# Kernel tuning notes

Hardware: AMD Instinct MI355X
Metric: run time of the kernel (lower is better)

The kernel has to match this reference:

```python
import jax, jax.numpy as jnp
import numpy as np

B, L, F, C, H, FF = 8, 64, 16, 128, 8, 512


def setup_inputs() -> dict:
    key = jax.random.key(0)
    ks = jax.random.split(key, 5)
    s = jnp.float32(0.02)
    return {
        "x": jax.random.normal(ks[0], (B, L, F, C), jnp.float32),
        "wq": jax.random.normal(ks[1], (C * H, C), jnp.float32) * s,
        "bq": jnp.zeros((C * H,), jnp.float32),
        "wk": jax.random.normal(ks[2], (C * H, C), jnp.float32) * s,
        "bk": jnp.zeros((C * H,), jnp.float32),
        "wv": jax.random.normal(ks[3], (C * H, C), jnp.float32) * s,
        "bv": jnp.zeros((C * H,), jnp.float32),
        "wo": jax.random.normal(ks[4], (C, C * H), jnp.float32) * s,
        "bo": jnp.zeros((C,), jnp.float32),
        "ln1_g": jnp.ones((C,), jnp.float32),
        "ln1_b": jnp.zeros((C,), jnp.float32),
        "w1": jax.random.normal(jax.random.fold_in(key, 10), (FF, C), jnp.float32) * s,
        "b1": jnp.zeros((FF,), jnp.float32),
        "w2": jax.random.normal(jax.random.fold_in(key, 11), (C, FF), jnp.float32) * s,
        "b2": jnp.zeros((C,), jnp.float32),
        "ln2_g": jnp.ones((C,), jnp.float32),
        "ln2_b": jnp.zeros((C,), jnp.float32),
    }


def _layer_norm(x, g, b, eps=1e-5):
    m = jnp.mean(x, axis=-1, keepdims=True)
    v = jnp.mean(jnp.square(x - m), axis=-1, keepdims=True)  # biased var, like torch LN
    return (x - m) * jax.lax.rsqrt(v + eps) * g + b


def reference(x, wq, bq, wk, bk, wv, bv, wo, bo, ln1_g, ln1_b, w1, b1, w2, b2, ln2_g, ln2_b):
    b_, l, f, c = x.shape
    h = wq.shape[0] // c  # num_heads

    def proj(w, bias):
        y = x @ w.T + bias                       # (B,L,F,C*H)
        y = y.reshape(b_, l, f, c, h)
        return jnp.transpose(y, (0, 4, 1, 2, 3))  # (B,H,L,F,C)

    q = proj(wq, bq)
    k = proj(wk, bk)
    v = proj(wv, bv)

    # scores over joint (L,F) query/key axes: (B,H,Lq,Fq,Lk,Fk)
    scores = jnp.einsum('bhlfc,bhmgc->bhlfmg', q, k) / jnp.sqrt(jnp.float32(c))
    # double softmax: first over key-L axis, then over key-F axis of the result
    a = jax.nn.softmax(scores, axis=4)
    a = jax.nn.softmax(a, axis=5)
    z = jnp.einsum('bhlfmg,bhmgc->bhlfc', a, v)   # (B,H,L,F,C)
    z = jnp.transpose(z, (0, 2, 3, 4, 1)).reshape(b_, l, f, c * h)
    attn_out = z @ wo.T + bo                      # (B,L,F,C)

    z1 = _layer_norm(attn_out + x, ln1_g, ln1_b)  # residual + LN1 (dropout=0, eval)
    ffy = jax.nn.relu(z1 @ w1.T + b1) @ w2.T + b2
    return _layer_norm(ffy + z1, ln2_g, ln2_b)
```

## Files before the change

kernel.cpp:

```cpp
#include <hip/hip_runtime.h>


typedef unsigned short u16;
typedef unsigned int u32;
typedef __attribute__((ext_vector_type(4))) float f32x4;
typedef __attribute__((ext_vector_type(8))) short s16x8;
typedef __attribute__((ext_vector_type(4))) unsigned short u16x4;

__device__ __forceinline__ u16 f2bf(float f) {
    union { float f; u32 u; } v; v.f = f;
    u32 u = v.u;
    u += 0x7fffu + ((u >> 16) & 1u);
    return (u16)(u >> 16);
}
__device__ __forceinline__ float bf2f(u16 h) {
    union { u32 u; float f; } v; v.u = ((u32)h) << 16;
    return v.f;
}
__device__ __forceinline__ u32 pack_trunc(float lo, float hi) {
    return __builtin_amdgcn_perm(__float_as_uint(hi), __float_as_uint(lo), 0x07060302u);
}
__device__ __forceinline__ s16x8 ldg8(const u16* p) { return *(const s16x8*)p; }

#define MFMA(a, b, c) __builtin_amdgcn_mfma_f32_16x16x32_bf16((a), (b), (c), 0, 0, 0)

__global__ __launch_bounds__(256) void k_prep(
    const float* __restrict__ x, const float* __restrict__ wq,
    const float* __restrict__ wk, const float* __restrict__ wv,
    const float* __restrict__ wo, const float* __restrict__ w1,
    const float* __restrict__ w2,
    u16* __restrict__ Xb, u16* __restrict__ Wqb, u16* __restrict__ Wkb,
    u16* __restrict__ Wvb, u16* __restrict__ Wob, u16* __restrict__ W1b,
    u16* __restrict__ W2b)
{
    int i = blockIdx.x * 256 + threadIdx.x;
    if (i < 360448) {
        int v = i * 4;
        float4 f; u16* dst; size_t addr;
        if (v < 1048576) {
            int t = v >> 7, k = v & 127;
            f = *(const float4*)(x + v);
            dst = Xb;
            addr = (size_t)((t >> 4) * 4 + (k >> 5)) * 512 + (t & 15) * 32 + (k & 31);
        } else {
            int v2 = v - 1048576;
            int w = v2 >> 17, off = v2 & 131071;
            const float* src = (w == 0) ? wq : (w == 1) ? wk : wv;
            dst = (w == 0) ? Wqb : (w == 1) ? Wkb : Wvb;
            int o = off >> 7, k = off & 127;
            int h = o & 7, cp = o >> 3;
            f = *(const float4*)(src + off);
            addr = (size_t)((h * 8 + (cp >> 4)) * 4 + (k >> 5)) * 512 + (cp & 15) * 32 + (k & 31);
        }
        u16x4 o4; o4.x = f2bf(f.x); o4.y = f2bf(f.y); o4.z = f2bf(f.z); o4.w = f2bf(f.w);
        *(u16x4*)(dst + addr) = o4;
    } else {
        int i2 = i - 360448;
        if (i2 < 131072) {
            int n = i2 >> 10, o2 = i2 & 1023;
            int h = o2 >> 7, c = o2 & 127;
            size_t addr = (size_t)((n >> 4) * 32 + (o2 >> 5)) * 512 + (n & 15) * 32 + (o2 & 31);
            Wob[addr] = f2bf(wo[n * 1024 + c * 8 + h]);
        } else {
            int v = (i2 - 131072) * 4;
            float4 f; u16* dst; size_t addr;
            if (v < 65536) {
                int o = v >> 7, k = v & 127;
                f = *(const float4*)(w1 + v);
                dst = W1b;
                addr = (size_t)((o >> 4) * 4 + (k >> 5)) * 512 + (o & 15) * 32 + (k & 31);
            } else {
                int v2 = v - 65536;
                int n = v2 >> 9, k = v2 & 511;
                f = *(const float4*)(w2 + v2);
                dst = W2b;
                addr = (size_t)((n >> 4) * 16 + (k >> 5)) * 512 + (n & 15) * 32 + (k & 31);
            }
            u16x4 o4; o4.x = f2bf(f.x); o4.y = f2bf(f.y); o4.z = f2bf(f.z); o4.w = f2bf(f.w);
            *(u16x4*)(dst + addr) = o4;
        }
    }
}

__global__ __launch_bounds__(256) void k_qkv(
    const u16* __restrict__ Xb,
    const u16* __restrict__ Wqb, const u16* __restrict__ Wkb, const u16* __restrict__ Wvb,
    const float* __restrict__ bq, const float* __restrict__ bk, const float* __restrict__ bv,
    u16* __restrict__ Qblk, u16* __restrict__ Kblk, u16* __restrict__ Vblk)
{
    const int tid = threadIdx.x, lane = tid & 63, wid = tid >> 6;
    const int colb = lane & 15, quad = lane >> 4;
    const int fl = colb * 32 + quad * 8;
    const int t0 = blockIdx.x * 128;
    const int cb = blockIdx.y;
    const int h = cb >> 1, c0 = (cb & 1) * 64;

    const u16* at0 = Xb + (size_t)((t0 >> 4) + wid * 2) * 2048 + fl;
    const u16* at1 = at0 + 2048;
    s16x8 a0[4], a1[4];
    #pragma unroll
    for (int i = 0; i < 4; ++i) { a0[i] = ldg8(at0 + i * 512); a1[i] = ldg8(at1 + i * 512); }

    #pragma unroll
    for (int gz = 0; gz < 3; ++gz) {
        const u16* W = (gz == 0) ? Wqb : (gz == 1) ? Wkb : Wvb;
        const float* bias = (gz == 0) ? bq : (gz == 1) ? bk : bv;
        f32x4 acc[2][4] = {};
        #pragma unroll
        for (int j = 0; j < 4; ++j) {
            int cpt = (c0 >> 4) + j;
            const u16* bt = W + (size_t)((h * 8 + cpt) * 4) * 512 + fl;
            #pragma unroll
            for (int i = 0; i < 4; ++i) {
                s16x8 b = ldg8(bt + i * 512);
                acc[0][j] = MFMA(a0[i], b, acc[0][j]);
                acc[1][j] = MFMA(a1[i], b, acc[1][j]);
            }
        }
        #pragma unroll
        for (int rt = 0; rt < 2; ++rt) {
            #pragma unroll
            for (int j = 0; j < 4; ++j) {
                int cpr = c0 + j * 16 + colb;
                float bs = bias[cpr * 8 + h];
                if (gz < 2) {
                    u16* dst = (gz == 0) ? Qblk : Kblk;
                    #pragma unroll
                    for (int r = 0; r < 4; ++r) {
                        int t = t0 + (wid * 2 + rt) * 16 + quad * 4 + r;
                        int bi = t >> 10, rr = t & 1023;
                        size_t addr = (size_t)(bi * 8 + h) * 131072
                                    + (size_t)((rr >> 4) * 4 + (cpr >> 5)) * 512
                                    + (rr & 15) * 32 + (cpr & 31);
                        dst[addr] = f2bf(acc[rt][j][r] + bs);
                    }
                } else {
                    int t = t0 + (wid * 2 + rt) * 16 + quad * 4;
                    int bi = t >> 10, rr = t & 1023;
                    size_t addr = (size_t)(bi * 8 + h) * 131072
                                + (size_t)((cpr >> 4) * 32 + (rr >> 5)) * 512
                                + (cpr & 15) * 32 + (rr & 31);
                    u16x4 o;
                    o.x = f2bf(acc[rt][j][0] + bs); o.y = f2bf(acc[rt][j][1] + bs);
                    o.z = f2bf(acc[rt][j][2] + bs); o.w = f2bf(acc[rt][j][3] + bs);
                    *(u16x4*)&Vblk[addr] = o;
                }
            }
        }
    }
}

__global__ __launch_bounds__(512, 4) void k_attn(
    const u16* __restrict__ Qblk, const u16* __restrict__ Kblk, const u16* __restrict__ Vblk,
    u16* __restrict__ Zblk)
{
    __shared__ u16 sS[32 * 1032];
    __shared__ float sZsum[32][16];
    __shared__ float sZi[32][20];

    const int tid = threadIdx.x, lane = tid & 63, wid = tid >> 6;
    const int colb = lane & 15, quad = lane >> 4;
    const int fl = colb * 32 + quad * 8;
    const int bid = blockIdx.x;
    const int bh = (bid & 7) + 8 * ((bid >> 3) & 7);
    const int r0 = (bid >> 6) * 32;
    const size_t qkb = (size_t)bh * 131072;
    const float SCALE = 0.08838834764831845f;

    sZsum[tid >> 4][tid & 15] = 0.f;
    __syncthreads();

    const u16* qt = Qblk + qkb + (size_t)(r0 >> 4) * 2048 + fl;
    s16x8 aq[2][4];
    #pragma unroll
    for (int mt = 0; mt < 2; ++mt)
        #pragma unroll
        for (int i = 0; i < 4; ++i)
            aq[mt][i] = ldg8(qt + mt * 2048 + i * 512);

    const u16* kt0 = Kblk + qkb + (size_t)wid * 2048 + fl;
    float zs[2][4] = {};
    s16x8 kc[4], kn[4];
    #pragma unroll
    for (int i = 0; i < 4; ++i) kc[i] = ldg8(kt0 + i * 512);
    #pragma unroll
    for (int j = 0; j < 8; ++j) {
        if (j < 7) {
            const u16* kp = kt0 + (size_t)(8 * (j + 1)) * 2048;
            #pragma unroll
            for (int i = 0; i < 4; ++i) kn[i] = ldg8(kp + i * 512);
        }
        f32x4 ac0 = {}, ac1 = {};
        ac0 = MFMA(aq[0][0], kc[0], ac0); ac1 = MFMA(aq[1][0], kc[0], ac1);
        ac0 = MFMA(aq[0][1], kc[1], ac0); ac1 = MFMA(aq[1][1], kc[1], ac1);
        ac0 = MFMA(aq[0][2], kc[2], ac0); ac1 = MFMA(aq[1][2], kc[2], ac1);
        ac0 = MFMA(aq[0][3], kc[3], ac0); ac1 = MFMA(aq[1][3], kc[3], ac1);
        const int kt = wid + 8 * j;
        #pragma unroll
        for (int r = 0; r < 4; ++r) {
            int row0 = quad * 4 + r;
            float p0 = __expf(ac0[r] * SCALE);
            float p1 = __expf(ac1[r] * SCALE);
            u32 u0 = __float_as_uint(p0), u1 = __float_as_uint(p1);
            zs[0][r] += __uint_as_float(u0 & 0xffff0000u);
            zs[1][r] += __uint_as_float(u1 & 0xffff0000u);
            sS[row0 * 1032 + kt * 16 + colb] = (u16)(u0 >> 16);
            sS[(16 + row0) * 1032 + kt * 16 + colb] = (u16)(u1 >> 16);
        }
        #pragma unroll
        for (int i = 0; i < 4; ++i) kc[i] = kn[i];
    }
    #pragma unroll
    for (int mt = 0; mt < 2; ++mt)
        #pragma unroll
        for (int r = 0; r < 4; ++r)
            atomicAdd(&sZsum[mt * 16 + quad * 4 + r][colb], zs[mt][r]);
    __syncthreads();

    {
        int row = tid >> 4, g = tid & 15;
        sZi[row][g] = 1.0f / sZsum[row][g];
    }
    __syncthreads();

    {
        const int row = tid & 31, mb = (tid >> 5) * 4;
        float zi[16];
        #pragma unroll
        for (int i = 0; i < 4; ++i) {
            f32x4 z4 = *(const f32x4*)&sZi[row][i * 4];
            zi[i*4] = z4[0]; zi[i*4+1] = z4[1]; zi[i*4+2] = z4[2]; zi[i*4+3] = z4[3];
        }
        #pragma unroll
        for (int tk = 0; tk < 4; ++tk) {
            int m = mb + tk;
            u16* base = &sS[row * 1032 + m * 16];
            s16x8 pa = *(const s16x8*)base;
            s16x8 pb = *(const s16x8*)(base + 8);
            float w[16]; float sum = 0.f;
            #pragma unroll
            for (int g = 0; g < 8; ++g) {
                w[g] = __expf(bf2f((u16)pa[g]) * zi[g]);      sum += w[g];
                w[g+8] = __expf(bf2f((u16)pb[g]) * zi[g+8]);  sum += w[g+8];
            }
            float inv = 1.0f / sum;
            u32 o[8];
            #pragma unroll
            for (int g = 0; g < 8; ++g)
                o[g] = pack_trunc(w[2*g] * inv, w[2*g+1] * inv);
            *(u32*)(base + 0)  = o[0]; *(u32*)(base + 2)  = o[1];
            *(u32*)(base + 4)  = o[2]; *(u32*)(base + 6)  = o[3];
            *(u32*)(base + 8)  = o[4]; *(u32*)(base + 10) = o[5];
            *(u32*)(base + 12) = o[6]; *(u32*)(base + 14) = o[7];
        }
    }
    __syncthreads();

    f32x4 zac[2] = {};
    const u16* aS0 = &sS[colb * 1032 + quad * 8];
    const u16* aS1 = aS0 + 16 * 1032;
    const u16* vt = Vblk + qkb + (size_t)wid * 16384 + fl;
    #pragma unroll
    for (int c = 0; c < 8; ++c) {
        s16x8 v[4];
        #pragma unroll
        for (int i = 0; i < 4; ++i) v[i] = ldg8(vt + (c * 4 + i) * 512);
        #pragma unroll
        for (int i = 0; i < 4; ++i) {
            int kk = (c * 4 + i) * 32;
            zac[0] = MFMA(*(const s16x8*)(aS0 + kk), v[i], zac[0]);
            zac[1] = MFMA(*(const s16x8*)(aS1 + kk), v[i], zac[1]);
        }
    }
    const int bi = bh >> 3, hh = bh & 7;
    const int tt = (bi * 1024 + r0) >> 4;
    #pragma unroll
    for (int mt = 0; mt < 2; ++mt) {
        size_t base = (size_t)((tt + mt) * 32 + hh * 4 + (wid >> 1)) * 512
                    + (wid & 1) * 16 + colb;
        #pragma unroll
        for (int r = 0; r < 4; ++r)
            Zblk[base + (quad * 4 + r) * 32] = f2bf(zac[mt][r]);
    }
}

__global__ __launch_bounds__(256) void k_tail(
    const u16* __restrict__ Zblk, const u16* __restrict__ Wob, const float* __restrict__ bo,
    const float* __restrict__ x,  const float* __restrict__ g1, const float* __restrict__ be1,
    const u16* __restrict__ W1b, const float* __restrict__ b1,
    const u16* __restrict__ W2b, const float* __restrict__ b2,
    const float* __restrict__ g2, const float* __restrict__ be2,
    float* __restrict__ out)
{
    __shared__ float sC[16][132];
    __shared__ float sZ1f[16][132];
    __shared__ u16  sZ1h[16][136];
    __shared__ u16  sH[16][520];
    const int tid = threadIdx.x, lane = tid & 63, w = tid >> 6;
    const int colb = lane & 15, quad = lane >> 4;
    const int fl = colb * 32 + quad * 8;
    const int t0 = blockIdx.x * 16;

    {
        const u16* at = Zblk + (size_t)blockIdx.x * 16384 + fl;
        f32x4 acc0 = {}, acc1 = {};
        const u16* bt0 = Wob + (size_t)(w * 2) * 16384 + fl;
        const u16* bt1 = bt0 + 16384;
        #pragma unroll
        for (int kt = 0; kt < 32; ++kt) {
            s16x8 a = ldg8(at + kt * 512);
            acc0 = MFMA(a, ldg8(bt0 + kt * 512), acc0);
            acc1 = MFMA(a, ldg8(bt1 + kt * 512), acc1);
        }
        #pragma unroll
        for (int r = 0; r < 4; ++r) {
            sC[quad * 4 + r][(w * 2) * 16 + colb] = acc0[r];
            sC[quad * 4 + r][(w * 2 + 1) * 16 + colb] = acc1[r];
        }
    }
    __syncthreads();

    {
        const int row = tid >> 4, cg = tid & 15;
        float v[8];
        {
            f32x4 s0 = *(const f32x4*)&sC[row][cg * 8];
            f32x4 s1 = *(const f32x4*)&sC[row][cg * 8 + 4];
            float4 x0 = *(const float4*)&x[(size_t)(t0 + row) * 128 + cg * 8];
            float4 x1 = *(const float4*)&x[(size_t)(t0 + row) * 128 + cg * 8 + 4];
            float4 b0 = *(const float4*)&bo[cg * 8];
            float4 b1v = *(const float4*)&bo[cg * 8 + 4];
            v[0] = s0[0]+b0.x+x0.x; v[1] = s0[1]+b0.y+x0.y;
            v[2] = s0[2]+b0.z+x0.z; v[3] = s0[3]+b0.w+x0.w;
            v[4] = s1[0]+b1v.x+x1.x; v[5] = s1[1]+b1v.y+x1.y;
            v[6] = s1[2]+b1v.z+x1.z; v[7] = s1[3]+b1v.w+x1.w;
        }
        float s = v[0]+v[1]+v[2]+v[3]+v[4]+v[5]+v[6]+v[7];
        s += __shfl_xor(s, 1); s += __shfl_xor(s, 2);
        s += __shfl_xor(s, 4); s += __shfl_xor(s, 8);
        float mean = s * (1.0f / 128.0f);
        float d, vs = 0.f;
        #pragma unroll
        for (int j = 0; j < 8; ++j) { d = v[j] - mean; vs += d * d; }
        vs += __shfl_xor(vs, 1); vs += __shfl_xor(vs, 2);
        vs += __shfl_xor(vs, 4); vs += __shfl_xor(vs, 8);
        float rstd = rsqrtf(vs * (1.0f / 128.0f) + 1e-5f);
        float4 gg0 = *(const float4*)&g1[cg * 8], gg1 = *(const float4*)&g1[cg * 8 + 4];
        float4 bb0 = *(const float4*)&be1[cg * 8], bb1 = *(const float4*)&be1[cg * 8 + 4];
        float z[8];
        z[0]=(v[0]-mean)*rstd*gg0.x+bb0.x; z[1]=(v[1]-mean)*rstd*gg0.y+bb0.y;
        z[2]=(v[2]-mean)*rstd*gg0.z+bb0.z; z[3]=(v[3]-mean)*rstd*gg0.w+bb0.w;
        z[4]=(v[4]-mean)*rstd*gg1.x+bb1.x; z[5]=(v[5]-mean)*rstd*gg1.y+bb1.y;
        z[6]=(v[6]-mean)*rstd*gg1.z+bb1.z; z[7]=(v[7]-mean)*rstd*gg1.w+bb1.w;
        *(f32x4*)&sZ1f[row][cg * 8]     = (f32x4){z[0], z[1], z[2], z[3]};
        *(f32x4*)&sZ1f[row][cg * 8 + 4] = (f32x4){z[4], z[5], z[6], z[7]};
        u16x4 h0, h1;
        h0.x=f2bf(z[0]); h0.y=f2bf(z[1]); h0.z=f2bf(z[2]); h0.w=f2bf(z[3]);
        h1.x=f2bf(z[4]); h1.y=f2bf(z[5]); h1.z=f2bf(z[6]); h1.w=f2bf(z[7]);
        *(u16x4*)&sZ1h[row][cg * 8] = h0;
        *(u16x4*)&sZ1h[row][cg * 8 + 4] = h1;
    }
    __syncthreads();

    {
        s16x8 bz[4];
        #pragma unroll
        for (int i = 0; i < 4; ++i)
            bz[i] = *(const s16x8*)&sZ1h[colb][quad * 8 + i * 32];
        #pragma unroll
        for (int ot = 0; ot < 8; ++ot) {
            const u16* wt = W1b + (size_t)((w * 8 + ot) * 4) * 512 + fl;
            f32x4 acc = {};
            acc = MFMA(ldg8(wt), bz[0], acc);
            acc = MFMA(ldg8(wt + 512), bz[1], acc);
            acc = MFMA(ldg8(wt + 1024), bz[2], acc);
            acc = MFMA(ldg8(wt + 1536), bz[3], acc);
            int o = w * 128 + ot * 16 + quad * 4;
            float4 bs = *(const float4*)&b1[o];
            u16x4 hv;
            hv.x = f2bf(fmaxf(acc[0] + bs.x, 0.f));
            hv.y = f2bf(fmaxf(acc[1] + bs.y, 0.f));
            hv.z = f2bf(fmaxf(acc[2] + bs.z, 0.f));
            hv.w = f2bf(fmaxf(acc[3] + bs.w, 0.f));
            *(u16x4*)&sH[colb][o] = hv;
        }
    }
    __syncthreads();

    {
        f32x4 acc0 = {}, acc1 = {};
        const u16* bt0 = W2b + (size_t)(w * 2) * 8192 + fl;
        const u16* bt1 = bt0 + 8192;
        #pragma unroll
        for (int kt = 0; kt < 16; ++kt) {
            s16x8 a = *(const s16x8*)&sH[colb][quad * 8 + kt * 32];
            acc0 = MFMA(a, ldg8(bt0 + kt * 512), acc0);
            acc1 = MFMA(a, ldg8(bt1 + kt * 512), acc1);
        }
        #pragma unroll
        for (int r = 0; r < 4; ++r) {
            sC[quad * 4 + r][(w * 2) * 16 + colb] = acc0[r];
            sC[quad * 4 + r][(w * 2 + 1) * 16 + colb] = acc1[r];
        }
    }
    __syncthreads();

    {
        const int row = tid >> 4, cg = tid & 15;
        float v[8];
        {
            f32x4 s0 = *(const f32x4*)&sC[row][cg * 8];
            f32x4 s1 = *(const f32x4*)&sC[row][cg * 8 + 4];
            f32x4 z0 = *(const f32x4*)&sZ1f[row][cg * 8];
            f32x4 z1 = *(const f32x4*)&sZ1f[row][cg * 8 + 4];
            float4 b0 = *(const float4*)&b2[cg * 8];
            float4 b1v = *(const float4*)&b2[cg * 8 + 4];
            v[0] = s0[0]+b0.x+z0[0]; v[1] = s0[1]+b0.y+z0[1];
            v[2] = s0[2]+b0.z+z0[2]; v[3] = s0[3]+b0.w+z0[3];
            v[4] = s1[0]+b1v.x+z1[0]; v[5] = s1[1]+b1v.y+z1[1];
            v[6] = s1[2]+b1v.z+z1[2]; v[7] = s1[3]+b1v.w+z1[3];
        }
        float s = v[0]+v[1]+v[2]+v[3]+v[4]+v[5]+v[6]+v[7];
        s += __shfl_xor(s, 1); s += __shfl_xor(s, 2);
        s += __shfl_xor(s, 4); s += __shfl_xor(s, 8);
        float mean = s * (1.0f / 128.0f);
        float d, vs = 0.f;
        #pragma unroll
        for (int j = 0; j < 8; ++j) { d = v[j] - mean; vs += d * d; }
        vs += __shfl_xor(vs, 1); vs += __shfl_xor(vs, 2);
        vs += __shfl_xor(vs, 4); vs += __shfl_xor(vs, 8);
        float rstd = rsqrtf(vs * (1.0f / 128.0f) + 1e-5f);
        float4 gg0 = *(const float4*)&g2[cg * 8], gg1 = *(const float4*)&g2[cg * 8 + 4];
        float4 bb0 = *(const float4*)&be2[cg * 8], bb1 = *(const float4*)&be2[cg * 8 + 4];
        size_t ob = (size_t)(t0 + row) * 128 + cg * 8;
        *(float4*)&out[ob] = make_float4(
            (v[0]-mean)*rstd*gg0.x+bb0.x, (v[1]-mean)*rstd*gg0.y+bb0.y,
            (v[2]-mean)*rstd*gg0.z+bb0.z, (v[3]-mean)*rstd*gg0.w+bb0.w);
        *(float4*)&out[ob + 4] = make_float4(
            (v[4]-mean)*rstd*gg1.x+bb1.x, (v[5]-mean)*rstd*gg1.y+bb1.y,
            (v[6]-mean)*rstd*gg1.z+bb1.z, (v[7]-mean)*rstd*gg1.w+bb1.w);
    }
}

extern "C" void kernel_launch(void* const* d_in, const int* in_sizes, int n_in,
                              void* d_out, int out_size, void* d_ws, size_t ws_size,
                              hipStream_t stream)
{
    (void)in_sizes; (void)n_in; (void)out_size; (void)ws_size;
    const float* x   = (const float*)d_in[0];
    const float* wq  = (const float*)d_in[1];
    const float* bq  = (const float*)d_in[2];
    const float* wk  = (const float*)d_in[3];
    const float* bk  = (const float*)d_in[4];
    const float* wv  = (const float*)d_in[5];
    const float* bv  = (const float*)d_in[6];
    const float* wo  = (const float*)d_in[7];
    const float* bo  = (const float*)d_in[8];
    const float* g1  = (const float*)d_in[9];
    const float* be1 = (const float*)d_in[10];
    const float* w1  = (const float*)d_in[11];
    const float* b1  = (const float*)d_in[12];
    const float* w2  = (const float*)d_in[13];
    const float* b2  = (const float*)d_in[14];
    const float* g2  = (const float*)d_in[15];
    const float* be2 = (const float*)d_in[16];

    char* ws = (char*)d_ws;
    const size_t MB = (size_t)1 << 20;
    u16*   Qblk = (u16*)(ws + 0 * MB);
    u16*   Kblk = (u16*)(ws + 16 * MB);
    u16*   Vblk = (u16*)(ws + 32 * MB);
    u16*   Zblk = (u16*)(ws + 48 * MB);
    u16*   Xb  = (u16*)(ws + 48 * MB);
    u16*   Wqb = (u16*)(ws + 50 * MB);
    u16*   Wkb = (u16*)(ws + 50 * MB + 262144);
    u16*   Wvb = (u16*)(ws + 50 * MB + 524288);
    u16*   Wob = (u16*)(ws + 64 * MB);
    u16*   W1b = (u16*)(ws + 64 * MB + 524288);
    u16*   W2b = (u16*)(ws + 64 * MB + 786432);
    float* out = (float*)d_out;

    k_prep<<<2048, 256, 0, stream>>>(x, wq, wk, wv, wo, w1, w2,
                                     Xb, Wqb, Wkb, Wvb, Wob, W1b, W2b);
    k_qkv<<<dim3(64, 16), 256, 0, stream>>>(Xb, Wqb, Wkb, Wvb, bq, bk, bv, Qblk, Kblk, Vblk);
    k_attn<<<2048, 512, 0, stream>>>(Qblk, Kblk, Vblk, Zblk);
    k_tail<<<512, 256, 0, stream>>>(Zblk, Wob, bo, x, g1, be1, W1b, b1, W2b, b2, g2, be2, out);
}
```

Before: 241.4 us.

## Halve attention query tile to 16 rows and double grid for occupancy

The attention kernel now processes 16 query rows per block instead of 32 and launches twice as many blocks. This halves LDS use (sS shrinks to 16 rows) and register pressure, so launch bounds can ask for 8 blocks per SM, and the explicit K prefetch double-buffering is removed. The cost is that each block reloads the same K and V tiles for half as many queries, which doubles K/V global and L2 traffic. Launch-bounds hints of 4 are also added to k_qkv and k_tail.

```diff
diff --git a/kernel.cpp b/kernel.cpp
--- a/kernel.cpp
+++ b/kernel.cpp
@@ -82,7 +82,7 @@
     }
 }
 
-__global__ __launch_bounds__(256) void k_qkv(
+__global__ __launch_bounds__(256, 4) void k_qkv(
     const u16* __restrict__ Xb,
     const u16* __restrict__ Wqb, const u16* __restrict__ Wkb, const u16* __restrict__ Wvb,
     const float* __restrict__ bq, const float* __restrict__ bk, const float* __restrict__ bv,
@@ -150,81 +150,62 @@
     }
 }
 
-__global__ __launch_bounds__(512, 4) void k_attn(
+__global__ __launch_bounds__(512, 8) void k_attn(
     const u16* __restrict__ Qblk, const u16* __restrict__ Kblk, const u16* __restrict__ Vblk,
     u16* __restrict__ Zblk)
 {
-    __shared__ u16 sS[32 * 1032];
-    __shared__ float sZsum[32][16];
-    __shared__ float sZi[32][20];
+    __shared__ u16 sS[16 * 1032];
+    __shared__ float sZsum[16][16];
+    __shared__ float sZi[16][20];
 
     const int tid = threadIdx.x, lane = tid & 63, wid = tid >> 6;
     const int colb = lane & 15, quad = lane >> 4;
     const int fl = colb * 32 + quad * 8;
     const int bid = blockIdx.x;
     const int bh = (bid & 7) + 8 * ((bid >> 3) & 7);
-    const int r0 = (bid >> 6) * 32;
+    const int r0 = (bid >> 6) * 16;
     const size_t qkb = (size_t)bh * 131072;
     const float SCALE = 0.08838834764831845f;
 
-    sZsum[tid >> 4][tid & 15] = 0.f;
+    if (tid < 256) sZsum[tid >> 4][tid & 15] = 0.f;
     __syncthreads();
 
     const u16* qt = Qblk + qkb + (size_t)(r0 >> 4) * 2048 + fl;
-    s16x8 aq[2][4];
-    #pragma unroll
-    for (int mt = 0; mt < 2; ++mt)
-        #pragma unroll
-        for (int i = 0; i < 4; ++i)
-            aq[mt][i] = ldg8(qt + mt * 2048 + i * 512);
+    s16x8 aq[4];
+    #pragma unroll
+    for (int i = 0; i < 4; ++i) aq[i] = ldg8(qt + i * 512);
 
     const u16* kt0 = Kblk + qkb + (size_t)wid * 2048 + fl;
-    float zs[2][4] = {};
-    s16x8 kc[4], kn[4];
-    #pragma unroll
-    for (int i = 0; i < 4; ++i) kc[i] = ldg8(kt0 + i * 512);
+    float zs[4] = {};
     #pragma unroll
     for (int j = 0; j < 8; ++j) {
-        if (j < 7) {
-            const u16* kp = kt0 + (size_t)(8 * (j + 1)) * 2048;
-            #pragma unroll
-            for (int i = 0; i < 4; ++i) kn[i] = ldg8(kp + i * 512);
-        }
-        f32x4 ac0 = {}, ac1 = {};
-        ac0 = MFMA(aq[0][0], kc[0], ac0); ac1 = MFMA(aq[1][0], kc[0], ac1);
-        ac0 = MFMA(aq[0][1], kc[1], ac0); ac1 = MFMA(aq[1][1], kc[1], ac1);
-        ac0 = MFMA(aq[0][2], kc[2], ac0); ac1 = MFMA(aq[1][2], kc[2], ac1);
-        ac0 = MFMA(aq[0][3], kc[3], ac0); ac1 = MFMA(aq[1][3], kc[3], ac1);
+        const u16* kp = kt0 + (size_t)(8 * j) * 2048;
+        s16x8 k0 = ldg8(kp), k1 = ldg8(kp + 512), k2 = ldg8(kp + 1024), k3 = ldg8(kp + 1536);
+        f32x4 ac = {};
+        ac = MFMA(aq[0], k0, ac);
+        ac = MFMA(aq[1], k1, ac);
+        ac = MFMA(aq[2], k2, ac);
+        ac = MFMA(aq[3], k3, ac);
         const int kt = wid + 8 * j;
         #pragma unroll
         for (int r = 0; r < 4; ++r) {
             int row0 = quad * 4 + r;
-            float p0 = __expf(ac0[r] * SCALE);
-            float p1 = __expf(ac1[r] * SCALE);
-            u32 u0 = __float_as_uint(p0), u1 = __float_as_uint(p1);
-            zs[0][r] += __uint_as_float(u0 & 0xffff0000u);
-            zs[1][r] += __uint_as_float(u1 & 0xffff0000u);
-            sS[row0 * 1032 + kt * 16 + colb] = (u16)(u0 >> 16);
-            sS[(16 + row0) * 1032 + kt * 16 + colb] = (u16)(u1 >> 16);
-        }
-        #pragma unroll
-        for (int i = 0; i < 4; ++i) kc[i] = kn[i];
-    }
-    #pragma unroll
-    for (int mt = 0; mt < 2; ++mt)
-        #pragma unroll
-        for (int r = 0; r < 4; ++r)
-            atomicAdd(&sZsum[mt * 16 + quad * 4 + r][colb], zs[mt][r]);
-    __syncthreads();
-
-    {
-        int row = tid >> 4, g = tid & 15;
-        sZi[row][g] = 1.0f / sZsum[row][g];
-    }
-    __syncthreads();
-
-    {
-        const int row = tid & 31, mb = (tid >> 5) * 4;
+            float p = __expf(ac[r] * SCALE);
+            u32 u = __float_as_uint(p);
+            zs[r] += __uint_as_float(u & 0xffff0000u);
+            sS[row0 * 1032 + kt * 16 + colb] = (u16)(u >> 16);
+        }
+    }
+    #pragma unroll
+    for (int r = 0; r < 4; ++r)
+        atomicAdd(&sZsum[quad * 4 + r][colb], zs[r]);
+    __syncthreads();
+
+    if (tid < 256) sZi[tid >> 4][tid & 15] = 1.0f / sZsum[tid >> 4][tid & 15];
+    __syncthreads();
+
+    {
+        const int row = tid & 15, mb = (tid >> 4) * 2;
         float zi[16];
         #pragma unroll
         for (int i = 0; i < 4; ++i) {
@@ -232,7 +213,7 @@
             zi[i*4] = z4[0]; zi[i*4+1] = z4[1]; zi[i*4+2] = z4[2]; zi[i*4+3] = z4[3];
         }
         #pragma unroll
-        for (int tk = 0; tk < 4; ++tk) {
+        for (int tk = 0; tk < 2; ++tk) {
             int m = mb + tk;
             u16* base = &sS[row * 1032 + m * 16];
             s16x8 pa = *(const s16x8*)base;
@@ -256,35 +237,30 @@
     }
     __syncthreads();
 
-    f32x4 zac[2] = {};
-    const u16* aS0 = &sS[colb * 1032 + quad * 8];
-    const u16* aS1 = aS0 + 16 * 1032;
+    f32x4 zac = {};
+    const u16* aS = &sS[colb * 1032 + quad * 8];
     const u16* vt = Vblk + qkb + (size_t)wid * 16384 + fl;
     #pragma unroll
     for (int c = 0; c < 8; ++c) {
-        s16x8 v[4];
-        #pragma unroll
-        for (int i = 0; i < 4; ++i) v[i] = ldg8(vt + (c * 4 + i) * 512);
-        #pragma unroll
-        for (int i = 0; i < 4; ++i) {
-            int kk = (c * 4 + i) * 32;
-            zac[0] = MFMA(*(const s16x8*)(aS0 + kk), v[i], zac[0]);
-            zac[1] = MFMA(*(const s16x8*)(aS1 + kk), v[i], zac[1]);
-        }
+        s16x8 v0 = ldg8(vt + (c * 4 + 0) * 512);
+        s16x8 v1 = ldg8(vt + (c * 4 + 1) * 512);
+        s16x8 v2 = ldg8(vt + (c * 4 + 2) * 512);
+        s16x8 v3 = ldg8(vt + (c * 4 + 3) * 512);
+        zac = MFMA(*(const s16x8*)(aS + (c * 4 + 0) * 32), v0, zac);
+        zac = MFMA(*(const s16x8*)(aS + (c * 4 + 1) * 32), v1, zac);
+        zac = MFMA(*(const s16x8*)(aS + (c * 4 + 2) * 32), v2, zac);
+        zac = MFMA(*(const s16x8*)(aS + (c * 4 + 3) * 32), v3, zac);
     }
     const int bi = bh >> 3, hh = bh & 7;
     const int tt = (bi * 1024 + r0) >> 4;
-    #pragma unroll
-    for (int mt = 0; mt < 2; ++mt) {
-        size_t base = (size_t)((tt + mt) * 32 + hh * 4 + (wid >> 1)) * 512
-                    + (wid & 1) * 16 + colb;
-        #pragma unroll
-        for (int r = 0; r < 4; ++r)
-            Zblk[base + (quad * 4 + r) * 32] = f2bf(zac[mt][r]);
-    }
-}
-
-__global__ __launch_bounds__(256) void k_tail(
+    size_t base = (size_t)(tt * 32 + hh * 4 + (wid >> 1)) * 512
+                + (wid & 1) * 16 + colb;
+    #pragma unroll
+    for (int r = 0; r < 4; ++r)
+        Zblk[base + (quad * 4 + r) * 32] = f2bf(zac[r]);
+}
+
+__global__ __launch_bounds__(256, 4) void k_tail(
     const u16* __restrict__ Zblk, const u16* __restrict__ Wob, const float* __restrict__ bo,
     const float* __restrict__ x,  const float* __restrict__ g1, const float* __restrict__ be1,
     const u16* __restrict__ W1b, const float* __restrict__ b1,
@@ -483,6 +459,6 @@
     k_prep<<<2048, 256, 0, stream>>>(x, wq, wk, wv, wo, w1, w2,
                                      Xb, Wqb, Wkb, Wvb, Wob, W1b, W2b);
     k_qkv<<<dim3(64, 16), 256, 0, stream>>>(Xb, Wqb, Wkb, Wvb, bq, bk, bv, Qblk, Kblk, Vblk);
-    k_attn<<<2048, 512, 0, stream>>>(Qblk, Kblk, Vblk, Zblk);
+    k_attn<<<4096, 512, 0, stream>>>(Qblk, Kblk, Vblk, Zblk);
     k_tail<<<512, 256, 0, stream>>>(Zblk, Wob, bo, x, g1, be1, W1b, b1, W2b, b2, g2, be2, out);
 }
```

New measurement: 266.5 us. 1.1x slower.

## Store attention probabilities as offset-encoded fp8 in LDS and add column-sum correction

Applied to the files above, without the earlier changes.

The attention kernel now keeps the intermediate exp-scores and the second-softmax probabilities in LDS as fp8 with affine offsets, instead of bf16. This halves shared memory per block so more blocks can be resident, and launch bounds are raised to 8 blocks. To undo the probability offset, k_qkv computes per-(batch,head) V column sums with atomics, and the output adds a vsum term. K loads lose their software prefetch, and the fp8 encoding risks accuracy loss; fp8 values are also widened back to bf16 in registers before the MFMA.

```diff
diff --git a/kernel.cpp b/kernel.cpp
--- a/kernel.cpp
+++ b/kernel.cpp
@@ -3,6 +3,7 @@
 
 typedef unsigned short u16;
 typedef unsigned int u32;
+typedef __attribute__((ext_vector_type(2))) float f32x2;
 typedef __attribute__((ext_vector_type(4))) float f32x4;
 typedef __attribute__((ext_vector_type(8))) short s16x8;
 typedef __attribute__((ext_vector_type(4))) unsigned short u16x4;
@@ -12,10 +13,6 @@
     u32 u = v.u;
     u += 0x7fffu + ((u >> 16) & 1u);
     return (u16)(u >> 16);
-}
-__device__ __forceinline__ float bf2f(u16 h) {
-    union { u32 u; float f; } v; v.u = ((u32)h) << 16;
-    return v.f;
 }
 __device__ __forceinline__ u32 pack_trunc(float lo, float hi) {
     return __builtin_amdgcn_perm(__float_as_uint(hi), __float_as_uint(lo), 0x07060302u);
@@ -31,7 +28,7 @@
     const float* __restrict__ w2,
     u16* __restrict__ Xb, u16* __restrict__ Wqb, u16* __restrict__ Wkb,
     u16* __restrict__ Wvb, u16* __restrict__ Wob, u16* __restrict__ W1b,
-    u16* __restrict__ W2b)
+    u16* __restrict__ W2b, float* __restrict__ Vcol)
 {
     int i = blockIdx.x * 256 + threadIdx.x;
     if (i < 360448) {
@@ -54,7 +51,7 @@
         }
         u16x4 o4; o4.x = f2bf(f.x); o4.y = f2bf(f.y); o4.z = f2bf(f.z); o4.w = f2bf(f.w);
         *(u16x4*)(dst + addr) = o4;
-    } else {
+    } else if (i < 524288) {
         int i2 = i - 360448;
         if (i2 < 131072) {
             int n = i2 >> 10, o2 = i2 & 1023;
@@ -79,6 +76,9 @@
             u16x4 o4; o4.x = f2bf(f.x); o4.y = f2bf(f.y); o4.z = f2bf(f.z); o4.w = f2bf(f.w);
             *(u16x4*)(dst + addr) = o4;
         }
+    } else {
+        int vz = i - 524288;
+        if (vz < 8192) Vcol[vz] = 0.f;
     }
 }
 
@@ -86,7 +86,8 @@
     const u16* __restrict__ Xb,
     const u16* __restrict__ Wqb, const u16* __restrict__ Wkb, const u16* __restrict__ Wvb,
     const float* __restrict__ bq, const float* __restrict__ bk, const float* __restrict__ bv,
-    u16* __restrict__ Qblk, u16* __restrict__ Kblk, u16* __restrict__ Vblk)
+    u16* __restrict__ Qblk, u16* __restrict__ Kblk, u16* __restrict__ Vblk,
+    float* __restrict__ Vcol)
 {
     const int tid = threadIdx.x, lane = tid & 63, wid = tid >> 6;
     const int colb = lane & 15, quad = lane >> 4;
@@ -94,6 +95,7 @@
     const int t0 = blockIdx.x * 128;
     const int cb = blockIdx.y;
     const int h = cb >> 1, c0 = (cb & 1) * 64;
+    const int bi = t0 >> 10;
 
     const u16* at0 = Xb + (size_t)((t0 >> 4) + wid * 2) * 2048 + fl;
     const u16* at1 = at0 + 2048;
@@ -128,7 +130,7 @@
                     #pragma unroll
                     for (int r = 0; r < 4; ++r) {
                         int t = t0 + (wid * 2 + rt) * 16 + quad * 4 + r;
-                        int bi = t >> 10, rr = t & 1023;
+                        int rr = t & 1023;
                         size_t addr = (size_t)(bi * 8 + h) * 131072
                                     + (size_t)((rr >> 4) * 4 + (cpr >> 5)) * 512
                                     + (rr & 15) * 32 + (cpr & 31);
@@ -136,7 +138,7 @@
                     }
                 } else {
                     int t = t0 + (wid * 2 + rt) * 16 + quad * 4;
-                    int bi = t >> 10, rr = t & 1023;
+                    int rr = t & 1023;
                     size_t addr = (size_t)(bi * 8 + h) * 131072
                                 + (size_t)((cpr >> 4) * 32 + (rr >> 5)) * 512
                                 + (cpr & 15) * 32 + (rr & 31);
@@ -144,19 +146,25 @@
                     o.x = f2bf(acc[rt][j][0] + bs); o.y = f2bf(acc[rt][j][1] + bs);
                     o.z = f2bf(acc[rt][j][2] + bs); o.w = f2bf(acc[rt][j][3] + bs);
                     *(u16x4*)&Vblk[addr] = o;
+                    float s = acc[rt][j][0] + acc[rt][j][1] + acc[rt][j][2] + acc[rt][j][3]
+                            + 4.0f * bs;
+                    s += __shfl_xor(s, 16);
+                    s += __shfl_xor(s, 32);
+                    if (quad == 0)
+                        atomicAdd(&Vcol[(bi * 8 + h) * 128 + cpr], s);
                 }
             }
         }
     }
 }
 
-__global__ __launch_bounds__(512, 4) void k_attn(
+__global__ __launch_bounds__(512, 8) void k_attn(
     const u16* __restrict__ Qblk, const u16* __restrict__ Kblk, const u16* __restrict__ Vblk,
-    u16* __restrict__ Zblk)
+    const float* __restrict__ Vcol, u16* __restrict__ Zblk)
 {
-    __shared__ u16 sS[32 * 1032];
+    __shared__ unsigned char sS8[32 * 1048];
     __shared__ float sZsum[32][16];
-    __shared__ float sZi[32][20];
+    __shared__ float sZi[32][17];
 
     const int tid = threadIdx.x, lane = tid & 63, wid = tid >> 6;
     const int colb = lane & 15, quad = lane >> 4;
@@ -180,35 +188,28 @@
 
     const u16* kt0 = Kblk + qkb + (size_t)wid * 2048 + fl;
     float zs[2][4] = {};
-    s16x8 kc[4], kn[4];
-    #pragma unroll
-    for (int i = 0; i < 4; ++i) kc[i] = ldg8(kt0 + i * 512);
     #pragma unroll
     for (int j = 0; j < 8; ++j) {
-        if (j < 7) {
-            const u16* kp = kt0 + (size_t)(8 * (j + 1)) * 2048;
-            #pragma unroll
-            for (int i = 0; i < 4; ++i) kn[i] = ldg8(kp + i * 512);
-        }
+        const u16* kp = kt0 + (size_t)(8 * j) * 2048;
+        s16x8 k0 = ldg8(kp), k1 = ldg8(kp + 512), k2 = ldg8(kp + 1024), k3 = ldg8(kp + 1536);
         f32x4 ac0 = {}, ac1 = {};
-        ac0 = MFMA(aq[0][0], kc[0], ac0); ac1 = MFMA(aq[1][0], kc[0], ac1);
-        ac0 = MFMA(aq[0][1], kc[1], ac0); ac1 = MFMA(aq[1][1], kc[1], ac1);
-        ac0 = MFMA(aq[0][2], kc[2], ac0); ac1 = MFMA(aq[1][2], kc[2], ac1);
-        ac0 = MFMA(aq[0][3], kc[3], ac0); ac1 = MFMA(aq[1][3], kc[3], ac1);
+        ac0 = MFMA(aq[0][0], k0, ac0); ac1 = MFMA(aq[1][0], k0, ac1);
+        ac0 = MFMA(aq[0][1], k1, ac0); ac1 = MFMA(aq[1][1], k1, ac1);
+        ac0 = MFMA(aq[0][2], k2, ac0); ac1 = MFMA(aq[1][2], k2, ac1);
+        ac0 = MFMA(aq[0][3], k3, ac0); ac1 = MFMA(aq[1][3], k3, ac1);
         const int kt = wid + 8 * j;
         #pragma unroll
         for (int r = 0; r < 4; ++r) {
             int row0 = quad * 4 + r;
             float p0 = __expf(ac0[r] * SCALE);
             float p1 = __expf(ac1[r] * SCALE);
-            u32 u0 = __float_as_uint(p0), u1 = __float_as_uint(p1);
-            zs[0][r] += __uint_as_float(u0 & 0xffff0000u);
-            zs[1][r] += __uint_as_float(u1 & 0xffff0000u);
-            sS[row0 * 1032 + kt * 16 + colb] = (u16)(u0 >> 16);
-            sS[(16 + row0) * 1032 + kt * 16 + colb] = (u16)(u1 >> 16);
-        }
-        #pragma unroll
-        for (int i = 0; i < 4; ++i) kc[i] = kn[i];
+            zs[0][r] += p0; zs[1][r] += p1;
+            float e0 = (p0 - 1.0f) * 8.0f;
+            float e1 = (p1 - 1.0f) * 8.0f;
+            u32 pk = (u32)__builtin_amdgcn_cvt_pk_fp8_f32(e0, e1, 0, false);
+            sS8[row0 * 1048 + kt * 16 + colb] = (unsigned char)(pk & 0xffu);
+            sS8[(16 + row0) * 1048 + kt * 16 + colb] = (unsigned char)((pk >> 8) & 0xffu);
+        }
     }
     #pragma unroll
     for (int mt = 0; mt < 2; ++mt)
@@ -217,74 +218,106 @@
             atomicAdd(&sZsum[mt * 16 + quad * 4 + r][colb], zs[mt][r]);
     __syncthreads();
 
-    {
-        int row = tid >> 4, g = tid & 15;
-        sZi[row][g] = 1.0f / sZsum[row][g];
-    }
+    sZi[tid >> 4][tid & 15] = 1.0f / sZsum[tid >> 4][tid & 15];
     __syncthreads();
 
     {
         const int row = tid & 31, mb = (tid >> 5) * 4;
         float zi[16];
         #pragma unroll
-        for (int i = 0; i < 4; ++i) {
-            f32x4 z4 = *(const f32x4*)&sZi[row][i * 4];
-            zi[i*4] = z4[0]; zi[i*4+1] = z4[1]; zi[i*4+2] = z4[2]; zi[i*4+3] = z4[3];
-        }
+        for (int g = 0; g < 16; ++g) zi[g] = sZi[row][g];
         #pragma unroll
         for (int tk = 0; tk < 4; ++tk) {
             int m = mb + tk;
-            u16* base = &sS[row * 1032 + m * 16];
-            s16x8 pa = *(const s16x8*)base;
-            s16x8 pb = *(const s16x8*)(base + 8);
+            u32* bp = (u32*)&sS8[row * 1048 + m * 16];
+            u32 w0 = bp[0], w1 = bp[1], w2 = bp[2], w3 = bp[3];
             float w[16]; float sum = 0.f;
             #pragma unroll
-            for (int g = 0; g < 8; ++g) {
-                w[g] = __expf(bf2f((u16)pa[g]) * zi[g]);      sum += w[g];
-                w[g+8] = __expf(bf2f((u16)pb[g]) * zi[g+8]);  sum += w[g+8];
+            for (int q4 = 0; q4 < 4; ++q4) {
+                u32 ww = (q4 == 0) ? w0 : (q4 == 1) ? w1 : (q4 == 2) ? w2 : w3;
+                f32x2 eA = __builtin_amdgcn_cvt_pk_f32_fp8(ww, false);
+                f32x2 eB = __builtin_amdgcn_cvt_pk_f32_fp8(ww, true);
+                int g = q4 * 4;
+                w[g+0] = __expf(zi[g+0] * fmaf(eA[0], 0.125f, 1.0f)); sum += w[g+0];
+                w[g+1] = __expf(zi[g+1] * fmaf(eA[1], 0.125f, 1.0f)); sum += w[g+1];
+                w[g+2] = __expf(zi[g+2] * fmaf(eB[0], 0.125f, 1.0f)); sum += w[g+2];
+                w[g+3] = __expf(zi[g+3] * fmaf(eB[1], 0.125f, 1.0f)); sum += w[g+3];
             }
-            float inv = 1.0f / sum;
-            u32 o[8];
-            #pragma unroll
-            for (int g = 0; g < 8; ++g)
-                o[g] = pack_trunc(w[2*g] * inv, w[2*g+1] * inv);
-            *(u32*)(base + 0)  = o[0]; *(u32*)(base + 2)  = o[1];
-            *(u32*)(base + 4)  = o[2]; *(u32*)(base + 6)  = o[3];
-            *(u32*)(base + 8)  = o[4]; *(u32*)(base + 10) = o[5];
-            *(u32*)(base + 12) = o[6]; *(u32*)(base + 14) = o[7];
+            float inv1024 = 1024.0f / sum;
+            u32 o0 = 0, o1 = 0, o2 = 0, o3 = 0;
+            o0 = (u32)__builtin_amdgcn_cvt_pk_fp8_f32(
+                     fmaf(w[0], inv1024, -64.f), fmaf(w[1], inv1024, -64.f), o0, false);
+            o0 = (u32)__builtin_amdgcn_cvt_pk_fp8_f32(
+                     fmaf(w[2], inv1024, -64.f), fmaf(w[3], inv1024, -64.f), o0, true);
+            o1 = (u32)__builtin_amdgcn_cvt_pk_fp8_f32(
+                     fmaf(w[4], inv1024, -64.f), fmaf(w[5], inv1024, -64.f), o1, false);
+            o1 = (u32)__builtin_amdgcn_cvt_pk_fp8_f32(
+                     fmaf(w[6], inv1024, -64.f), fmaf(w[7], inv1024, -64.f), o1, true);
+            o2 = (u32)__builtin_amdgcn_cvt_pk_fp8_f32(
+                     fmaf(w[8], inv1024, -64.f), fmaf(w[9], inv1024, -64.f), o2, false);
+            o2 = (u32)__builtin_amdgcn_cvt_pk_fp8_f32(
+                     fmaf(w[10], inv1024, -64.f), fmaf(w[11], inv1024, -64.f), o2, true);
+            o3 = (u32)__builtin_amdgcn_cvt_pk_fp8_f32(
+                     fmaf(w[12], inv1024, -64.f), fmaf(w[13], inv1024, -64.f), o3, false);
+            o3 = (u32)__builtin_amdgcn_cvt_pk_fp8_f32(
+                     fmaf(w[14], inv1024, -64.f), fmaf(w[15], inv1024, -64.f), o3, true);
+            bp[0] = o0; bp[1] = o1; bp[2] = o2; bp[3] = o3;
         }
     }
     __syncthreads();
 
     f32x4 zac[2] = {};
-    const u16* aS0 = &sS[colb * 1032 + quad * 8];
-    const u16* aS1 = aS0 + 16 * 1032;
+    const unsigned char* aS0 = &sS8[colb * 1048 + quad * 8];
+    const unsigned char* aS1 = aS0 + 16 * 1048;
     const u16* vt = Vblk + qkb + (size_t)wid * 16384 + fl;
     #pragma unroll
     for (int c = 0; c < 8; ++c) {
-        s16x8 v[4];
-        #pragma unroll
-        for (int i = 0; i < 4; ++i) v[i] = ldg8(vt + (c * 4 + i) * 512);
         #pragma unroll
         for (int i = 0; i < 4; ++i) {
             int kk = (c * 4 + i) * 32;
-            zac[0] = MFMA(*(const s16x8*)(aS0 + kk), v[i], zac[0]);
-            zac[1] = MFMA(*(const s16x8*)(aS1 + kk), v[i], zac[1]);
+            s16x8 v = ldg8(vt + (c * 4 + i) * 512);
+            const u32* pa0 = (const u32*)(aS0 + kk);
+            const u32* pa1 = (const u32*)(aS1 + kk);
+            u32 a0lo = pa0[0], a0hi = pa0[1];
+            u32 a1lo = pa1[0], a1hi = pa1[1];
+            f32x2 f0 = __builtin_amdgcn_cvt_pk_f32_fp8(a0lo, false);
+            f32x2 f1 = __builtin_amdgcn_cvt_pk_f32_fp8(a0lo, true);
+            f32x2 f2 = __builtin_amdgcn_cvt_pk_f32_fp8(a0hi, false);
+            f32x2 f3 = __builtin_amdgcn_cvt_pk_f32_fp8(a0hi, true);
+            s16x8 s0;
+            *((u32*)&s0 + 0) = pack_trunc(f0[0], f0[1]);
+            *((u32*)&s0 + 1) = pack_trunc(f1[0], f1[1]);
+            *((u32*)&s0 + 2) = pack_trunc(f2[0], f2[1]);
+            *((u32*)&s0 + 3) = pack_trunc(f3[0], f3[1]);
+            f32x2 g0 = __builtin_amdgcn_cvt_pk_f32_fp8(a1lo, false);
+            f32x2 g1 = __builtin_amdgcn_cvt_pk_f32_fp8(a1lo, true);
+            f32x2 g2 = __builtin_amdgcn_cvt_pk_f32_fp8(a1hi, false);
+            f32x2 g3 = __builtin_amdgcn_cvt_pk_f32_fp8(a1hi, true);
+            s16x8 s1;
+            *((u32*)&s1 + 0) = pack_trunc(g0[0], g0[1]);
+            *((u32*)&s1 + 1) = pack_trunc(g1[0], g1[1]);
+            *((u32*)&s1 + 2) = pack_trunc(g2[0], g2[1]);
+            *((u32*)&s1 + 3) = pack_trunc(g3[0], g3[1]);
+            zac[0] = MFMA(s0, v, zac[0]);
+            zac[1] = MFMA(s1, v, zac[1]);
         }
     }
     const int bi = bh >> 3, hh = bh & 7;
     const int tt = (bi * 1024 + r0) >> 4;
+    const float vsum = Vcol[bh * 128 + wid * 16 + colb];
     #pragma unroll
     for (int mt = 0; mt < 2; ++mt) {
         size_t base = (size_t)((tt + mt) * 32 + hh * 4 + (wid >> 1)) * 512
                     + (wid & 1) * 16 + colb;
         #pragma unroll
-        for (int r = 0; r < 4; ++r)
-            Zblk[base + (quad * 4 + r) * 32] = f2bf(zac[mt][r]);
-    }
-}
-
-__global__ __launch_bounds__(256) void k_tail(
+        for (int r = 0; r < 4; ++r) {
+            float z = fmaf(zac[mt][r], 0.0009765625f, vsum * 0.0625f);
+            Zblk[base + (quad * 4 + r) * 32] = f2bf(z);
+        }
+    }
+}
+
+__global__ __launch_bounds__(256, 4) void k_tail(
     const u16* __restrict__ Zblk, const u16* __restrict__ Wob, const float* __restrict__ bo,
     const float* __restrict__ x,  const float* __restrict__ g1, const float* __restrict__ be1,
     const u16* __restrict__ W1b, const float* __restrict__ b1,
@@ -475,14 +508,16 @@
     u16*   Wqb = (u16*)(ws + 50 * MB);
     u16*   Wkb = (u16*)(ws + 50 * MB + 262144);
     u16*   Wvb = (u16*)(ws + 50 * MB + 524288);
-    u16*   Wob = (u16*)(ws + 64 * MB);
-    u16*   W1b = (u16*)(ws + 64 * MB + 524288);
-    u16*   W2b = (u16*)(ws + 64 * MB + 786432);
+    u16*   Wob  = (u16*)(ws + 64 * MB);
+    u16*   W1b  = (u16*)(ws + 64 * MB + 524288);
+    u16*   W2b  = (u16*)(ws + 64 * MB + 786432);
+    float* Vcol = (float*)(ws + 65 * MB);
     float* out = (float*)d_out;
 
-    k_prep<<<2048, 256, 0, stream>>>(x, wq, wk, wv, wo, w1, w2,
-                                     Xb, Wqb, Wkb, Wvb, Wob, W1b, W2b);
-    k_qkv<<<dim3(64, 16), 256, 0, stream>>>(Xb, Wqb, Wkb, Wvb, bq, bk, bv, Qblk, Kblk, Vblk);
-    k_attn<<<2048, 512, 0, stream>>>(Qblk, Kblk, Vblk, Zblk);
+    k_prep<<<2080, 256, 0, stream>>>(x, wq, wk, wv, wo, w1, w2,
+                                     Xb, Wqb, Wkb, Wvb, Wob, W1b, W2b, Vcol);
+    k_qkv<<<dim3(64, 16), 256, 0, stream>>>(Xb, Wqb, Wkb, Wvb, bq, bk, bv,
+                                            Qblk, Kblk, Vblk, Vcol);
+    k_attn<<<2048, 512, 0, stream>>>(Qblk, Kblk, Vblk, Vcol, Zblk);
     k_tail<<<512, 256, 0, stream>>>(Zblk, Wob, bo, x, g1, be1, W1b, b1, W2b, b2, g2, be2, out);
 }
```

Measured after the change: 286.4 us. 1.19x slower.

## Process 32 tokens per tail block to reuse weight fragments across two tiles

Applied to the files above, without the earlier changes.

Each k_tail block now handles 32 tokens with 512 threads instead of 16 tokens with 256. Each wave loads one weight fragment and applies it to two token tiles in the Wo, W1 and W2 GEMMs. This halves the global weight traffic per token. In exchange the grid halves to 256 blocks and shared memory per block doubles, which may cut latency hiding.

```diff
diff --git a/kernel.cpp b/kernel.cpp
--- a/kernel.cpp
+++ b/kernel.cpp
@@ -284,7 +284,7 @@
     }
 }
 
-__global__ __launch_bounds__(256) void k_tail(
+__global__ __launch_bounds__(512, 2) void k_tail(
     const u16* __restrict__ Zblk, const u16* __restrict__ Wob, const float* __restrict__ bo,
     const float* __restrict__ x,  const float* __restrict__ g1, const float* __restrict__ be1,
     const u16* __restrict__ W1b, const float* __restrict__ b1,
@@ -292,30 +292,30 @@
     const float* __restrict__ g2, const float* __restrict__ be2,
     float* __restrict__ out)
 {
-    __shared__ float sC[16][132];
-    __shared__ float sZ1f[16][132];
-    __shared__ u16  sZ1h[16][136];
-    __shared__ u16  sH[16][520];
+    __shared__ float sC[32][132];
+    __shared__ float sZ1f[32][132];
+    __shared__ u16  sZ1h[32][136];
+    __shared__ u16  sH[32][520];
     const int tid = threadIdx.x, lane = tid & 63, w = tid >> 6;
     const int colb = lane & 15, quad = lane >> 4;
     const int fl = colb * 32 + quad * 8;
-    const int t0 = blockIdx.x * 16;
-
-    {
-        const u16* at = Zblk + (size_t)blockIdx.x * 16384 + fl;
+    const int t0 = blockIdx.x * 32;
+
+    {
+        const u16* at0 = Zblk + (size_t)(blockIdx.x * 2) * 16384 + fl;
+        const u16* at1 = at0 + 16384;
+        const u16* bt = Wob + (size_t)w * 16384 + fl;
         f32x4 acc0 = {}, acc1 = {};
-        const u16* bt0 = Wob + (size_t)(w * 2) * 16384 + fl;
-        const u16* bt1 = bt0 + 16384;
         #pragma unroll
         for (int kt = 0; kt < 32; ++kt) {
-            s16x8 a = ldg8(at + kt * 512);
-            acc0 = MFMA(a, ldg8(bt0 + kt * 512), acc0);
-            acc1 = MFMA(a, ldg8(bt1 + kt * 512), acc1);
+            s16x8 b = ldg8(bt + kt * 512);
+            acc0 = MFMA(ldg8(at0 + kt * 512), b, acc0);
+            acc1 = MFMA(ldg8(at1 + kt * 512), b, acc1);
         }
         #pragma unroll
         for (int r = 0; r < 4; ++r) {
-            sC[quad * 4 + r][(w * 2) * 16 + colb] = acc0[r];
-            sC[quad * 4 + r][(w * 2 + 1) * 16 + colb] = acc1[r];
+            sC[quad * 4 + r][w * 16 + colb] = acc0[r];
+            sC[16 + quad * 4 + r][w * 16 + colb] = acc1[r];
         }
     }
     __syncthreads();
@@ -363,44 +363,54 @@
     __syncthreads();
 
     {
-        s16x8 bz[4];
-        #pragma unroll
-        for (int i = 0; i < 4; ++i)
-            bz[i] = *(const s16x8*)&sZ1h[colb][quad * 8 + i * 32];
-        #pragma unroll
-        for (int ot = 0; ot < 8; ++ot) {
-            const u16* wt = W1b + (size_t)((w * 8 + ot) * 4) * 512 + fl;
-            f32x4 acc = {};
-            acc = MFMA(ldg8(wt), bz[0], acc);
-            acc = MFMA(ldg8(wt + 512), bz[1], acc);
-            acc = MFMA(ldg8(wt + 1024), bz[2], acc);
-            acc = MFMA(ldg8(wt + 1536), bz[3], acc);
-            int o = w * 128 + ot * 16 + quad * 4;
+        s16x8 bz0[4], bz1[4];
+        #pragma unroll
+        for (int i = 0; i < 4; ++i) {
+            bz0[i] = *(const s16x8*)&sZ1h[colb][quad * 8 + i * 32];
+            bz1[i] = *(const s16x8*)&sZ1h[16 + colb][quad * 8 + i * 32];
+        }
+        #pragma unroll
+        for (int ot = 0; ot < 4; ++ot) {
+            const u16* wt = W1b + (size_t)((w * 4 + ot) * 4) * 512 + fl;
+            s16x8 wf0 = ldg8(wt), wf1 = ldg8(wt + 512);
+            s16x8 wf2 = ldg8(wt + 1024), wf3 = ldg8(wt + 1536);
+            f32x4 a0 = {}, a1 = {};
+            a0 = MFMA(wf0, bz0[0], a0); a1 = MFMA(wf0, bz1[0], a1);
+            a0 = MFMA(wf1, bz0[1], a0); a1 = MFMA(wf1, bz1[1], a1);
+            a0 = MFMA(wf2, bz0[2], a0); a1 = MFMA(wf2, bz1[2], a1);
+            a0 = MFMA(wf3, bz0[3], a0); a1 = MFMA(wf3, bz1[3], a1);
+            int o = (w * 4 + ot) * 16 + quad * 4;
             float4 bs = *(const float4*)&b1[o];
-            u16x4 hv;
-            hv.x = f2bf(fmaxf(acc[0] + bs.x, 0.f));
-            hv.y = f2bf(fmaxf(acc[1] + bs.y, 0.f));
-            hv.z = f2bf(fmaxf(acc[2] + bs.z, 0.f));
-            hv.w = f2bf(fmaxf(acc[3] + bs.w, 0.f));
-            *(u16x4*)&sH[colb][o] = hv;
-        }
-    }
-    __syncthreads();
-
-    {
+            u16x4 hv0, hv1;
+            hv0.x = f2bf(fmaxf(a0[0] + bs.x, 0.f));
+            hv0.y = f2bf(fmaxf(a0[1] + bs.y, 0.f));
+            hv0.z = f2bf(fmaxf(a0[2] + bs.z, 0.f));
+            hv0.w = f2bf(fmaxf(a0[3] + bs.w, 0.f));
+            hv1.x = f2bf(fmaxf(a1[0] + bs.x, 0.f));
+            hv1.y = f2bf(fmaxf(a1[1] + bs.y, 0.f));
+            hv1.z = f2bf(fmaxf(a1[2] + bs.z, 0.f));
+            hv1.w = f2bf(fmaxf(a1[3] + bs.w, 0.f));
+            *(u16x4*)&sH[colb][o] = hv0;
+            *(u16x4*)&sH[16 + colb][o] = hv1;
+        }
+    }
+    __syncthreads();
+
+    {
+        const u16* bt = W2b + (size_t)w * 8192 + fl;
         f32x4 acc0 = {}, acc1 = {};
-        const u16* bt0 = W2b + (size_t)(w * 2) * 8192 + fl;
-        const u16* bt1 = bt0 + 8192;
         #pragma unroll
         for (int kt = 0; kt < 16; ++kt) {
-            s16x8 a = *(const s16x8*)&sH[colb][quad * 8 + kt * 32];
-            acc0 = MFMA(a, ldg8(bt0 + kt * 512), acc0);
-            acc1 = MFMA(a, ldg8(bt1 + kt * 512), acc1);
+            s16x8 b = ldg8(bt + kt * 512);
+            s16x8 a0 = *(const s16x8*)&sH[colb][quad * 8 + kt * 32];
+            s16x8 a1 = *(const s16x8*)&sH[16 + colb][quad * 8 + kt * 32];
+            acc0 = MFMA(a0, b, acc0);
+            acc1 = MFMA(a1, b, acc1);
         }
         #pragma unroll
         for (int r = 0; r < 4; ++r) {
-            sC[quad * 4 + r][(w * 2) * 16 + colb] = acc0[r];
-            sC[quad * 4 + r][(w * 2 + 1) * 16 + colb] = acc1[r];
+            sC[quad * 4 + r][w * 16 + colb] = acc0[r];
+            sC[16 + quad * 4 + r][w * 16 + colb] = acc1[r];
         }
     }
     __syncthreads();
@@ -484,5 +494,5 @@
                                      Xb, Wqb, Wkb, Wvb, Wob, W1b, W2b);
     k_qkv<<<dim3(64, 16), 256, 0, stream>>>(Xb, Wqb, Wkb, Wvb, bq, bk, bv, Qblk, Kblk, Vblk);
     k_attn<<<2048, 512, 0, stream>>>(Qblk, Kblk, Vblk, Zblk);
-    k_tail<<<512, 256, 0, stream>>>(Zblk, Wob, bo, x, g1, be1, W1b, b1, W2b, b2, g2, be2, out);
-}
+    k_tail<<<256, 512, 0, stream>>>(Zblk, Wob, bo, x, g1, be1, W1b, b1, W2b, b2, g2, be2, out);
+}
```

Result: no change. 240.1 us (-0.5%).
